# Performance work log

Measured on AMD Instinct MI355X. Metric: run time of the kernel, lower is better.

The kernel has to match this reference:

```python
import jax, jax.numpy as jnp
import numpy as np

B, R, NM, H, P1, G1, RC1, LAT = 16384, 360, 200, 256, 512, 256, 256, 128


def _linear_params(k, out_f, in_f):
    s = 1.0 / np.sqrt(in_f)
    kw, kb = jax.random.split(k)
    W = jax.random.uniform(kw, (out_f, in_f), minval=-s, maxval=s, dtype=jnp.float32)
    b = jax.random.uniform(kb, (out_f,), minval=-s, maxval=s, dtype=jnp.float32)
    return W, b


def setup_inputs() -> dict:
    key = jax.random.key(0)
    ks = jax.random.split(key, 14)
    x_window = jax.random.normal(ks[0], (B, 3, R), dtype=jnp.float32)
    modes = jax.random.normal(ks[1], (R, NM), dtype=jnp.float32)
    mode_coeff = jax.random.normal(ks[2], (B, NM), dtype=jnp.float32)
    W1, b1 = _linear_params(ks[3], H, 3 * R)      # surrogate layer 1
    W2, b2 = _linear_params(ks[4], H, H)          # surrogate layer 2
    W3, b3 = _linear_params(ks[5], R, H)          # surrogate layer 3
    Wp1, bp1 = _linear_params(ks[6], P1, R * R)   # npi_proj
    Wp2, bp2 = _linear_params(ks[7], LAT, P1)
    Wg1, bg1 = _linear_params(ks[8], G1, NM)      # geo_proj
    Wg2, bg2 = _linear_params(ks[9], LAT, G1)
    Wr1, br1 = _linear_params(ks[10], RC1, LAT)   # recon
    Wr2, br2 = _linear_params(ks[11], R, RC1)
    return dict(x_window=x_window, modes=modes, mode_coeff=mode_coeff,
                W1=W1, b1=b1, W2=W2, b2=b2, W3=W3, b3=b3,
                Wp1=Wp1, bp1=bp1, Wp2=Wp2, bp2=bp2,
                Wg1=Wg1, bg1=bg1, Wg2=Wg2, bg2=bg2,
                Wr1=Wr1, br1=br1, Wr2=Wr2, br2=br2)


def reference(x_window, modes, mode_coeff,
              W1, b1, W2, b2, W3, b3,
              Wp1, bp1, Wp2, bp2,
              Wg1, bg1, Wg2, bg2,
              Wr1, br1, Wr2, br2):
    Bs = x_window.shape[0]
    Rr = W3.shape[0]
    # ---- NPI surrogate forward (needed for ReLU masks) ----
    z = x_window.reshape(Bs, 3 * Rr)                       # (B, 3R)
    h1 = z @ W1.T + b1                                     # (B, H)
    m1 = (h1 > 0).astype(z.dtype)
    h2 = (h1 * m1) @ W2.T + b2                             # (B, H)
    m2 = (h2 > 0).astype(z.dtype)
    # ---- EC: exact batch-mean Jacobian of the ReLU MLP w.r.t last timestep ----
    # mean_b [ W3 diag(m2_b) W2 diag(m1_b) W1_last ] = W3 @ (W2 * (m2^T m1 / B)) @ W1[:, -R:]
    G = (m2.T @ m1) / Bs                                   # (H, H)
    ec = W3 @ ((W2 * G) @ W1[:, -Rr:])                     # (R, R); row j = dy_j/dx
    ec = jax.lax.stop_gradient(ec)                         # create_graph=False in original
    # ---- projections ----
    ec_flat = ec.reshape(1, Rr * Rr)
    z_npi1 = jax.nn.relu(ec_flat @ Wp1.T + bp1) @ Wp2.T + bp2   # (1, LAT)
    z_npi = jnp.tile(z_npi1, (Bs, 1))                           # (B, LAT)
    z_geo = jax.nn.relu(mode_coeff @ Wg1.T + bg1) @ Wg2.T + bg2  # (B, LAT)
    zsum = z_npi + z_geo
    zn = zsum / jnp.maximum(jnp.linalg.norm(zsum, axis=-1, keepdims=True), 1e-12)
    recon = jax.nn.relu(zn @ Wr1.T + br1) @ Wr2.T + br2          # (B, R)
    return (z_npi, z_geo, zn, ec, recon)
```

## Files before the change

### kernel.cpp

```cpp
#include <hip/hip_runtime.h>

typedef __bf16 bf16x8 __attribute__((ext_vector_type(8)));
typedef __bf16 bf16x4 __attribute__((ext_vector_type(4)));
typedef float  f32x4  __attribute__((ext_vector_type(4)));

__device__ __forceinline__ f32x4 mfma_bf16(bf16x8 a, bf16x8 b, f32x4 c) {
  return __builtin_amdgcn_mfma_f32_16x16x32_bf16(a, b, c, 0, 0, 0);
}
__device__ __forceinline__ bf16x8 ldB(const __bf16* Bp, int kt, int NT, int nt,
                                      int lane) {
  return *reinterpret_cast<const bf16x8*>(Bp + (((size_t)kt * NT + nt) * 64 + lane) * 8);
}

__device__ __forceinline__ void gridbar(int* cnt, int target) {
  __syncthreads();
  if (threadIdx.x == 0) {
    __threadfence();
    __hip_atomic_fetch_add(cnt, 1, __ATOMIC_RELEASE, __HIP_MEMORY_SCOPE_AGENT);
    while (__hip_atomic_load(cnt, __ATOMIC_RELAXED, __HIP_MEMORY_SCOPE_AGENT) < target)
      __builtin_amdgcn_s_sleep(4);
    __threadfence();
  }
  __syncthreads();
}

__global__ void pack_all(const float* __restrict__ W1, const float* __restrict__ W2,
                         const float* __restrict__ Wg1, const float* __restrict__ Wg2,
                         const float* __restrict__ Wr1, const float* __restrict__ Wr2,
                         __bf16* __restrict__ W1p, __bf16* __restrict__ W2p,
                         __bf16* __restrict__ Wg1p, __bf16* __restrict__ Wg2p,
                         __bf16* __restrict__ Wr1p, __bf16* __restrict__ Wr2p,
                         float* __restrict__ G, int* __restrict__ cnt) {
  int bx = blockIdx.x;
  int lane = threadIdx.x;
  if (bx >= 1104) {
    if (bx == 1104 && lane == 0) cnt[0] = 0;
    float4* g = (float4*)G;
    int base = (bx - 1104) * 512 + lane;
#pragma unroll
    for (int i = 0; i < 8; ++i) g[base + i * 64] = make_float4(0.f, 0.f, 0.f, 0.f);
    return;
  }
  const float* W; __bf16* out; int N, K, NT, local;
  if (bx < 544)      { W = W1;  out = W1p;  N = 256; K = 1080; NT = 16; local = bx; }
  else if (bx < 672) { W = W2;  out = W2p;  N = 256; K = 256;  NT = 16; local = bx - 544; }
  else if (bx < 784) { W = Wg1; out = Wg1p; N = 256; K = 200;  NT = 16; local = bx - 672; }
  else if (bx < 848) { W = Wg2; out = Wg2p; N = 128; K = 256;  NT = 8;  local = bx - 784; }
  else if (bx < 912) { W = Wr1; out = Wr1p; N = 256; K = 128;  NT = 16; local = bx - 848; }
  else               { W = Wr2; out = Wr2p; N = 360; K = 256;  NT = 24; local = bx - 912; }
  int nt = local % NT, kt = local / NT;
  int n = nt * 16 + (lane & 15);
  int k0 = kt * 32 + (lane >> 4) * 8;
  bf16x8 v;
#pragma unroll
  for (int e = 0; e < 8; ++e) {
    int k = k0 + e;
    float xv = (n < N && k < K) ? W[(size_t)n * K + k] : 0.f;
    v[e] = (__bf16)xv;
  }
  *reinterpret_cast<bf16x8*>(out + ((size_t)local * 64 + lane) * 8) = v;
}

__global__ __launch_bounds__(512) void h1h2_fused(
    const float* __restrict__ x, const __bf16* __restrict__ W1p,
    const float* __restrict__ b1, const __bf16* __restrict__ W2p,
    const float* __restrict__ b2, __bf16* __restrict__ m1T,
    __bf16* __restrict__ m2T) {
  __shared__ __bf16 Alds[32][68];
  __shared__ __bf16 h1s[32][264];
  int tid = threadIdx.x;
  int lane = tid & 63, wid = tid >> 6;
  int wr = wid >> 2, wc = wid & 3;
  int rowBase = blockIdx.x * 32;
  int sr = tid >> 4, sc = (tid & 15) * 4;
  const float* aSrc = x + (size_t)(rowBase + sr) * 1080;
  f32x4 acc[4] = {};
  float4 c0, c1;
  auto LD = [&](int s, float4& d) {
    int gk = s * 64 + sc;
    d = (gk < 1080) ? *(const float4*)(aSrc + gk) : make_float4(0.f, 0.f, 0.f, 0.f);
  };
  LD(0, c0);
  LD(1, c1);
  for (int s = 0; s < 17; ++s) {
    bf16x4 w4;
    w4[0] = (__bf16)c0.x; w4[1] = (__bf16)c0.y;
    w4[2] = (__bf16)c0.z; w4[3] = (__bf16)c0.w;
    *reinterpret_cast<bf16x4*>(&Alds[sr][sc]) = w4;
    __syncthreads();
    c0 = c1;
    if (s + 2 < 17) LD(s + 2, c1);
    int arow = wr * 16 + (lane & 15);
#pragma unroll
    for (int ks = 0; ks < 2; ++ks) {
      int ak = ks * 32 + (lane >> 4) * 8;
      bf16x8 a0 = *reinterpret_cast<const bf16x8*>(&Alds[arow][ak]);
      int kt = s * 2 + ks;
#pragma unroll
      for (int n = 0; n < 4; ++n) {
        bf16x8 bv = ldB(W1p, kt, 16, wc * 4 + n, lane);
        acc[n] = mfma_bf16(a0, bv, acc[n]);
      }
    }
    __syncthreads();
  }
  int q4 = (lane >> 4) * 4;
#pragma unroll
  for (int n = 0; n < 4; ++n) {
    int col = wc * 64 + n * 16 + (lane & 15);
    float bb = b1[col];
#pragma unroll
    for (int j = 0; j < 4; ++j) {
      int rl = wr * 16 + q4 + j;
      float h = acc[n][j] + bb;
      m1T[(size_t)col * 16384 + rowBase + rl] = (__bf16)(h > 0.f ? 1.f : 0.f);
      h1s[rl][col] = (__bf16)fmaxf(h, 0.f);
    }
  }
  __syncthreads();
  f32x4 acc2[4] = {};
#pragma unroll
  for (int ks = 0; ks < 8; ++ks) {
    int arow = wr * 16 + (lane & 15), ak = ks * 32 + (lane >> 4) * 8;
    bf16x8 a0 = *reinterpret_cast<const bf16x8*>(&h1s[arow][ak]);
#pragma unroll
    for (int n = 0; n < 4; ++n) {
      bf16x8 bv = ldB(W2p, ks, 16, wc * 4 + n, lane);
      acc2[n] = mfma_bf16(a0, bv, acc2[n]);
    }
  }
#pragma unroll
  for (int n = 0; n < 4; ++n) {
    int col = wc * 64 + n * 16 + (lane & 15);
    float bb = b2[col];
#pragma unroll
    for (int j = 0; j < 4; ++j) {
      int rl = wr * 16 + q4 + j;
      float h = acc2[n][j] + bb;
      m2T[(size_t)col * 16384 + rowBase + rl] = (__bf16)(h > 0.f ? 1.f : 0.f);
    }
  }
}

__global__ __launch_bounds__(256) void gemm_masks(
    const __bf16* __restrict__ m2T, const __bf16* __restrict__ m1T,
    float* __restrict__ G) {
  int tid = threadIdx.x;
  int lane = tid & 63, wid = tid >> 6;
  int wr = wid >> 1, wc = wid & 1;
  int ibase = blockIdx.x * 64, jbase = blockIdx.y * 64;
  size_t b0 = (size_t)blockIdx.z * 1024 + (lane >> 4) * 8;
  const __bf16* pa0 = m2T + (size_t)(ibase + wr * 32 + (lane & 15)) * 16384 + b0;
  const __bf16* pa1 = pa0 + (size_t)16 * 16384;
  const __bf16* pb0 = m1T + (size_t)(jbase + wc * 32 + (lane & 15)) * 16384 + b0;
  const __bf16* pb1 = pb0 + (size_t)16 * 16384;
  f32x4 acc[2][2] = {};
#pragma unroll 4
  for (int c = 0; c < 32; ++c) {
    bf16x8 a0 = *reinterpret_cast<const bf16x8*>(pa0 + c * 32);
    bf16x8 a1 = *reinterpret_cast<const bf16x8*>(pa1 + c * 32);
    bf16x8 bv0 = *reinterpret_cast<const bf16x8*>(pb0 + c * 32);
    bf16x8 bv1 = *reinterpret_cast<const bf16x8*>(pb1 + c * 32);
    acc[0][0] = mfma_bf16(a0, bv0, acc[0][0]);
    acc[0][1] = mfma_bf16(a0, bv1, acc[0][1]);
    acc[1][0] = mfma_bf16(a1, bv0, acc[1][0]);
    acc[1][1] = mfma_bf16(a1, bv1, acc[1][1]);
  }
  int q4 = (lane >> 4) * 4;
#pragma unroll
  for (int m = 0; m < 2; ++m)
#pragma unroll
    for (int n = 0; n < 2; ++n)
#pragma unroll
      for (int j = 0; j < 4; ++j) {
        int gi = ibase + wr * 32 + m * 16 + q4 + j;
        int gj = jbase + wc * 32 + n * 16 + (lane & 15);
        atomicAdd(&G[(size_t)gi * 256 + gj], acc[m][n][j] * (1.f / 16384.f));
      }
}

__device__ void small_body2(float (*As)[17], float (*Bs)[65], int t,
                            const float* __restrict__ A, const float* __restrict__ A2,
                            int lda, const float* __restrict__ Bm, int ldb,
                            bool sum4, size_t bStride, float* __restrict__ C,
                            int ldc, int M, int N, int kBeg, int kEnd,
                            int m0, int n0) {
  int tx = t & 15, ty = t >> 4;
  float acc[4][4] = {};
  for (int k0 = kBeg; k0 < kEnd; k0 += 16) {
#pragma unroll
    for (int i = 0; i < 4; ++i) {
      int idx = t * 4 + i;
      int r = idx >> 4, kk = idx & 15;
      int gm = m0 + r, gk = k0 + kk;
      float v = (gm < M) ? A[(size_t)gm * lda + gk] : 0.f;
      if (A2 && gm < M) v *= A2[(size_t)gm * lda + gk];
      As[r][kk] = v;
      int kk2 = idx >> 6, cc = idx & 63;
      int gk2 = k0 + kk2, gn = n0 + cc;
      float bv = 0.f;
      if (gn < N) {
        const float* bp = Bm + (size_t)gk2 * ldb + gn;
        bv = bp[0];
        if (sum4) bv = bv + bp[bStride] + bp[2 * bStride] + bp[3 * bStride];
      }
      Bs[kk2][cc] = bv;
    }
    __syncthreads();
#pragma unroll
    for (int kk = 0; kk < 16; ++kk)
#pragma unroll
      for (int i = 0; i < 4; ++i)
#pragma unroll
        for (int j = 0; j < 4; ++j)
          acc[i][j] += As[ty * 4 + i][kk] * Bs[kk][tx * 4 + j];
    __syncthreads();
  }
#pragma unroll
  for (int i = 0; i < 4; ++i)
#pragma unroll
    for (int j = 0; j < 4; ++j) {
      int gm = m0 + ty * 4 + i, gn = n0 + tx * 4 + j;
      if (gm < M && gn < N) C[(size_t)gm * ldc + gn] = acc[i][j];
    }
}

__global__ __launch_bounds__(256) void small_split(
    const float* __restrict__ W2, const float* __restrict__ G,
    const float* __restrict__ W1, const float* __restrict__ W3,
    float* __restrict__ Tpart, float* __restrict__ ecpart,
    float* __restrict__ o_ec, int* __restrict__ cnt) {
  __shared__ float As[64][17];
  __shared__ float Bs[16][65];
  int t = threadIdx.x, bid = blockIdx.x;
  if (bid < 96) {
    int tile = bid >> 2, kc = bid & 3;
    small_body2(As, Bs, t, W2, G, 256, W1 + 720, 1080, false, 0,
                Tpart + (size_t)kc * 98304, 384, 256, 360,
                kc * 64, kc * 64 + 64, (tile / 6) * 64, (tile % 6) * 64);
  }
  gridbar(cnt, 144);
  {
    int tile = bid >> 2, kc = bid & 3;
    small_body2(As, Bs, t, W3, nullptr, 256, Tpart, 384, true, 98304,
                ecpart + (size_t)kc * 129600, 360, 360, 360,
                kc * 64, kc * 64 + 64, (tile / 6) * 64, (tile % 6) * 64);
  }
  gridbar(cnt, 288);
  {
    int base = bid * 900;
    for (int i = t; i < 900; i += 256) {
      int idx = base + i;
      o_ec[idx] = ecpart[idx] + ecpart[129600 + idx] + ecpart[259200 + idx] +
                  ecpart[388800 + idx];
    }
  }
}

__global__ __launch_bounds__(512) void p_and_g1(
    const float* __restrict__ Wp1, const float* __restrict__ ec,
    const float* __restrict__ bp1, float* __restrict__ p,
    const float* __restrict__ mc, const __bf16* __restrict__ Wg1p,
    const float* __restrict__ bg1, const __bf16* __restrict__ Wg2p,
    const float* __restrict__ bg2, float* __restrict__ o_zgeo) {
  __shared__ __bf16 Alds[64][40];
  __shared__ __bf16 g1S[64][264];
  __shared__ float redw[8];
  int t = threadIdx.x;
  if (blockIdx.x < 512) {
    int row = blockIdx.x;
    const float4* w = (const float4*)(Wp1 + (size_t)row * 129600);
    const float4* e = (const float4*)ec;
    float s = 0.f;
    for (int i = t; i < 32400; i += 512) {
      float4 a = w[i], b = e[i];
      s += a.x * b.x + a.y * b.y + a.z * b.z + a.w * b.w;
    }
    for (int o = 32; o; o >>= 1) s += __shfl_down(s, o);
    if ((t & 63) == 0) redw[t >> 6] = s;
    __syncthreads();
    if (t == 0) {
      float tot = 0.f;
#pragma unroll
      for (int i = 0; i < 8; ++i) tot += redw[i];
      p[row] = fmaxf(tot + bp1[row], 0.f);
    }
  } else {
    int lane = t & 63, wid = t >> 6;
    int wr = wid >> 2, wc = wid & 3;
    int rowBase = (blockIdx.x - 512) * 64;
    int sr = t >> 3, sc = (t & 7) * 4;
    const float* aSrc = mc + (size_t)(rowBase + sr) * 200;
    int q4 = (lane >> 4) * 4;
    f32x4 acc[2][4] = {};
    for (int kt = 0; kt < 7; ++kt) {
      int gk = kt * 32 + sc;
      bf16x4 w4;
      if (gk < 200) {
        float4 v = *(const float4*)(aSrc + gk);
        w4[0] = (__bf16)v.x; w4[1] = (__bf16)v.y;
        w4[2] = (__bf16)v.z; w4[3] = (__bf16)v.w;
      } else {
        w4[0] = w4[1] = w4[2] = w4[3] = (__bf16)0.f;
      }
      *reinterpret_cast<bf16x4*>(&Alds[sr][sc]) = w4;
      __syncthreads();
      int arow = wr * 32 + (lane & 15), ak = (lane >> 4) * 8;
      bf16x8 a0 = *reinterpret_cast<const bf16x8*>(&Alds[arow][ak]);
      bf16x8 a1 = *reinterpret_cast<const bf16x8*>(&Alds[arow + 16][ak]);
#pragma unroll
      for (int n = 0; n < 4; ++n) {
        bf16x8 bv = ldB(Wg1p, kt, 16, wc * 4 + n, lane);
        acc[0][n] = mfma_bf16(a0, bv, acc[0][n]);
        acc[1][n] = mfma_bf16(a1, bv, acc[1][n]);
      }
      __syncthreads();
    }
#pragma unroll
    for (int m = 0; m < 2; ++m)
#pragma unroll
      for (int n = 0; n < 4; ++n) {
        int col = wc * 64 + n * 16 + (lane & 15);
        float bb = bg1[col];
#pragma unroll
        for (int j = 0; j < 4; ++j) {
          int rl = wr * 32 + m * 16 + q4 + j;
          g1S[rl][col] = (__bf16)fmaxf(acc[m][n][j] + bb, 0.f);
        }
      }
    __syncthreads();
    f32x4 acc2[2][2] = {};
#pragma unroll
    for (int ks = 0; ks < 8; ++ks) {
      int arow = wr * 32 + (lane & 15), ak = ks * 32 + (lane >> 4) * 8;
      bf16x8 a0 = *reinterpret_cast<const bf16x8*>(&g1S[arow][ak]);
      bf16x8 a1 = *reinterpret_cast<const bf16x8*>(&g1S[arow + 16][ak]);
#pragma unroll
      for (int n = 0; n < 2; ++n) {
        bf16x8 bv = ldB(Wg2p, ks, 8, wc * 2 + n, lane);
        acc2[0][n] = mfma_bf16(a0, bv, acc2[0][n]);
        acc2[1][n] = mfma_bf16(a1, bv, acc2[1][n]);
      }
    }
#pragma unroll
    for (int m = 0; m < 2; ++m)
#pragma unroll
      for (int n = 0; n < 2; ++n) {
        int col = wc * 32 + n * 16 + (lane & 15);
        float bb = bg2[col];
#pragma unroll
        for (int j = 0; j < 4; ++j) {
          int row = rowBase + wr * 32 + m * 16 + q4 + j;
          o_zgeo[(size_t)row * 128 + col] = acc2[m][n][j] + bb;
        }
      }
  }
}

__global__ void gemv_z(const float* __restrict__ p, const float* __restrict__ Wp2,
                       const float* __restrict__ bp2, float* __restrict__ znpi1) {
  int j = blockIdx.x;
  int t = threadIdx.x;
  const float4* w = (const float4*)(Wp2 + (size_t)j * 512);
  const float4* pp = (const float4*)p;
  float4 a0 = w[t], b0 = pp[t];
  float4 a1 = w[t + 64], b1 = pp[t + 64];
  float s = a0.x * b0.x + a0.y * b0.y + a0.z * b0.z + a0.w * b0.w +
            a1.x * b1.x + a1.y * b1.y + a1.z * b1.z + a1.w * b1.w;
  for (int o = 32; o; o >>= 1) s += __shfl_down(s, o);
  if (t == 0) znpi1[j] = s + bp2[j];
}

__global__ __launch_bounds__(512) void mega_tail(
    const float* __restrict__ zgeo, const float* __restrict__ znpi1,
    const __bf16* __restrict__ Wr1p, const float* __restrict__ br1,
    const __bf16* __restrict__ Wr2p, const float* __restrict__ br2,
    float* __restrict__ o_znpi, float* __restrict__ o_zn,
    float* __restrict__ o_rec) {
  __shared__ __bf16 r1S[64][264];
  __shared__ __bf16 znS[64][136];
  __shared__ float znpiS[128];
  int tid = threadIdx.x;
  int lane = tid & 63, wid = tid >> 6;
  int wr = wid >> 2, wc = wid & 3;
  int rowBase = blockIdx.x * 64;
  int q4 = (lane >> 4) * 4;
  if (tid < 128) znpiS[tid] = znpi1[tid];
  __syncthreads();
  {
    int rg = tid >> 5;
    int c4 = (tid & 31) * 4;
    float4 zp = make_float4(znpiS[c4], znpiS[c4 + 1], znpiS[c4 + 2], znpiS[c4 + 3]);
#pragma unroll
    for (int ri = 0; ri < 4; ++ri) {
      int rl = rg + ri * 16;
      int row = rowBase + rl;
      float4 zg = *(const float4*)(zgeo + (size_t)row * 128 + c4);
      float4 zs = make_float4(zg.x + zp.x, zg.y + zp.y, zg.z + zp.z, zg.w + zp.w);
      *(float4*)(o_znpi + (size_t)row * 128 + c4) = zp;
      float ss = zs.x * zs.x + zs.y * zs.y + zs.z * zs.z + zs.w * zs.w;
      ss += __shfl_xor(ss, 1);
      ss += __shfl_xor(ss, 2);
      ss += __shfl_xor(ss, 4);
      ss += __shfl_xor(ss, 8);
      ss += __shfl_xor(ss, 16);
      float rn = 1.f / fmaxf(sqrtf(ss), 1e-12f);
      float4 zn = make_float4(zs.x * rn, zs.y * rn, zs.z * rn, zs.w * rn);
      *(float4*)(o_zn + (size_t)row * 128 + c4) = zn;
      bf16x4 znb;
      znb[0] = (__bf16)zn.x; znb[1] = (__bf16)zn.y;
      znb[2] = (__bf16)zn.z; znb[3] = (__bf16)zn.w;
      *reinterpret_cast<bf16x4*>(&znS[rl][c4]) = znb;
    }
  }
  __syncthreads();
  {
    f32x4 acc[2][4] = {};
#pragma unroll
    for (int ks = 0; ks < 4; ++ks) {
      int arow = wr * 32 + (lane & 15), ak = ks * 32 + (lane >> 4) * 8;
      bf16x8 a0 = *reinterpret_cast<const bf16x8*>(&znS[arow][ak]);
      bf16x8 a1 = *reinterpret_cast<const bf16x8*>(&znS[arow + 16][ak]);
#pragma unroll
      for (int n = 0; n < 4; ++n) {
        bf16x8 bv = ldB(Wr1p, ks, 16, wc * 4 + n, lane);
        acc[0][n] = mfma_bf16(a0, bv, acc[0][n]);
        acc[1][n] = mfma_bf16(a1, bv, acc[1][n]);
      }
    }
#pragma unroll
    for (int m = 0; m < 2; ++m)
#pragma unroll
      for (int n = 0; n < 4; ++n) {
        int col = wc * 64 + n * 16 + (lane & 15);
        float bb = br1[col];
#pragma unroll
        for (int j = 0; j < 4; ++j) {
          int rl = wr * 32 + m * 16 + q4 + j;
          r1S[rl][col] = (__bf16)fmaxf(acc[m][n][j] + bb, 0.f);
        }
      }
  }
  __syncthreads();
  {
    f32x4 acc[2][6] = {};
#pragma unroll
    for (int ks = 0; ks < 8; ++ks) {
      int arow = wr * 32 + (lane & 15), ak = ks * 32 + (lane >> 4) * 8;
      bf16x8 a0 = *reinterpret_cast<const bf16x8*>(&r1S[arow][ak]);
      bf16x8 a1 = *reinterpret_cast<const bf16x8*>(&r1S[arow + 16][ak]);
#pragma unroll
      for (int n = 0; n < 6; ++n) {
        bf16x8 bv = ldB(Wr2p, ks, 24, wc * 6 + n, lane);
        acc[0][n] = mfma_bf16(a0, bv, acc[0][n]);
        acc[1][n] = mfma_bf16(a1, bv, acc[1][n]);
      }
    }
#pragma unroll
    for (int m = 0; m < 2; ++m)
#pragma unroll
      for (int n = 0; n < 6; ++n) {
        int col = wc * 96 + n * 16 + (lane & 15);
        if (col < 360) {
          float bb = br2[col];
#pragma unroll
          for (int j = 0; j < 4; ++j) {
            int rl = wr * 32 + m * 16 + q4 + j;
            o_rec[(size_t)(rowBase + rl) * 360 + col] = acc[m][n][j] + bb;
          }
        }
      }
  }
}

extern "C" void kernel_launch(void* const* d_in, const int* in_sizes, int n_in,
                              void* d_out, int out_size, void* d_ws,
                              size_t ws_size, hipStream_t stream) {
  (void)in_sizes; (void)n_in; (void)out_size; (void)ws_size;
  const float* x   = (const float*)d_in[0];
  const float* mc  = (const float*)d_in[2];
  const float* W1  = (const float*)d_in[3];  const float* b1  = (const float*)d_in[4];
  const float* W2  = (const float*)d_in[5];  const float* b2  = (const float*)d_in[6];
  const float* W3  = (const float*)d_in[7];
  const float* Wp1 = (const float*)d_in[9];  const float* bp1 = (const float*)d_in[10];
  const float* Wp2 = (const float*)d_in[11]; const float* bp2 = (const float*)d_in[12];
  const float* Wg1 = (const float*)d_in[13]; const float* bg1 = (const float*)d_in[14];
  const float* Wg2 = (const float*)d_in[15]; const float* bg2 = (const float*)d_in[16];
  const float* Wr1 = (const float*)d_in[17]; const float* br1 = (const float*)d_in[18];
  const float* Wr2 = (const float*)d_in[19]; const float* br2 = (const float*)d_in[20];

  float* out = (float*)d_out;
  float* o_znpi = out;
  float* o_zgeo = out + 2097152;
  float* o_zn   = out + 4194304;
  float* o_ec   = out + 6291456;
  float* o_rec  = out + 6421056;

  char* ws = (char*)d_ws;
  __bf16* m1T    = (__bf16*)(ws + 0);
  __bf16* m2T    = (__bf16*)(ws + 8388608);
  float*  G      = (float*)(ws + 16777216);
  float*  Tpart  = (float*)(ws + 17039360);
  float*  ecpart = (float*)(ws + 18612224);
  float*  p512   = (float*)(ws + 20686848);
  float*  znpi1  = (float*)(ws + 20688896);
  __bf16* W1p    = (__bf16*)(ws + 20689920);
  __bf16* W2p    = W1p  + (size_t)544 * 512;
  __bf16* Wg1p   = W2p  + (size_t)128 * 512;
  __bf16* Wg2p   = Wg1p + (size_t)112 * 512;
  __bf16* Wr1p   = Wg2p + (size_t)64 * 512;
  __bf16* Wr2p   = Wr1p + (size_t)64 * 512;
  int*    cnt    = (int*)(ws + 22020096);

  pack_all<<<1136, 64, 0, stream>>>(W1, W2, Wg1, Wg2, Wr1, Wr2,
                                    W1p, W2p, Wg1p, Wg2p, Wr1p, Wr2p, G, cnt);
  h1h2_fused<<<512, 512, 0, stream>>>(x, W1p, b1, W2p, b2, m1T, m2T);
  gemm_masks<<<dim3(4, 4, 16), 256, 0, stream>>>(m2T, m1T, G);
  small_split<<<144, 256, 0, stream>>>(W2, G, W1, W3, Tpart, ecpart, o_ec, cnt);
  p_and_g1<<<768, 512, 0, stream>>>(Wp1, o_ec, bp1, p512, mc, Wg1p, bg1,
                                    Wg2p, bg2, o_zgeo);
  gemv_z<<<128, 64, 0, stream>>>(p512, Wp2, bp2, znpi1);
  mega_tail<<<256, 512, 0, stream>>>(o_zgeo, znpi1, Wr1p, br1, Wr2p, br2,
                                     o_znpi, o_zn, o_rec);
}
```

Baseline: 221.6 us.

## Fuse mask GEMM into EC kernel and fold Wp2 GEMV into last p block

The separate gemm_masks launch is merged into the EC kernel as a first phase, with an extra grid barrier before the small GEMM phases; the grid grows to 256 blocks. The gemv_z kernel is removed, and the last-finishing block of the Wp1 projection, found through an atomic counter, computes the 128-output GEMV. This removes two kernel launches and their gaps. The cost is an extra grid-wide barrier, and the design relies on all 256 blocks being co-resident and on a second counter reset in pack_all.

```diff
diff --git a/kernel.cpp b/kernel.cpp
--- a/kernel.cpp
+++ b/kernel.cpp
@@ -34,7 +34,7 @@
   int bx = blockIdx.x;
   int lane = threadIdx.x;
   if (bx >= 1104) {
-    if (bx == 1104 && lane == 0) cnt[0] = 0;
+    if (bx == 1104 && lane < 2) cnt[lane] = 0;
     float4* g = (float4*)G;
     int base = (bx - 1104) * 512 + lane;
 #pragma unroll
@@ -142,43 +142,6 @@
   }
 }
 
-__global__ __launch_bounds__(256) void gemm_masks(
-    const __bf16* __restrict__ m2T, const __bf16* __restrict__ m1T,
-    float* __restrict__ G) {
-  int tid = threadIdx.x;
-  int lane = tid & 63, wid = tid >> 6;
-  int wr = wid >> 1, wc = wid & 1;
-  int ibase = blockIdx.x * 64, jbase = blockIdx.y * 64;
-  size_t b0 = (size_t)blockIdx.z * 1024 + (lane >> 4) * 8;
-  const __bf16* pa0 = m2T + (size_t)(ibase + wr * 32 + (lane & 15)) * 16384 + b0;
-  const __bf16* pa1 = pa0 + (size_t)16 * 16384;
-  const __bf16* pb0 = m1T + (size_t)(jbase + wc * 32 + (lane & 15)) * 16384 + b0;
-  const __bf16* pb1 = pb0 + (size_t)16 * 16384;
-  f32x4 acc[2][2] = {};
-#pragma unroll 4
-  for (int c = 0; c < 32; ++c) {
-    bf16x8 a0 = *reinterpret_cast<const bf16x8*>(pa0 + c * 32);
-    bf16x8 a1 = *reinterpret_cast<const bf16x8*>(pa1 + c * 32);
-    bf16x8 bv0 = *reinterpret_cast<const bf16x8*>(pb0 + c * 32);
-    bf16x8 bv1 = *reinterpret_cast<const bf16x8*>(pb1 + c * 32);
-    acc[0][0] = mfma_bf16(a0, bv0, acc[0][0]);
-    acc[0][1] = mfma_bf16(a0, bv1, acc[0][1]);
-    acc[1][0] = mfma_bf16(a1, bv0, acc[1][0]);
-    acc[1][1] = mfma_bf16(a1, bv1, acc[1][1]);
-  }
-  int q4 = (lane >> 4) * 4;
-#pragma unroll
-  for (int m = 0; m < 2; ++m)
-#pragma unroll
-    for (int n = 0; n < 2; ++n)
-#pragma unroll
-      for (int j = 0; j < 4; ++j) {
-        int gi = ibase + wr * 32 + m * 16 + q4 + j;
-        int gj = jbase + wc * 32 + n * 16 + (lane & 15);
-        atomicAdd(&G[(size_t)gi * 256 + gj], acc[m][n][j] * (1.f / 16384.f));
-      }
-}
-
 __device__ void small_body2(float (*As)[17], float (*Bs)[65], int t,
                             const float* __restrict__ A, const float* __restrict__ A2,
                             int lda, const float* __restrict__ Bm, int ldb,
@@ -225,31 +188,68 @@
     }
 }
 
-__global__ __launch_bounds__(256) void small_split(
-    const float* __restrict__ W2, const float* __restrict__ G,
-    const float* __restrict__ W1, const float* __restrict__ W3,
+__global__ __launch_bounds__(256) void masks_ec(
+    const __bf16* __restrict__ m2T, const __bf16* __restrict__ m1T,
+    float* __restrict__ G,
+    const float* __restrict__ W2, const float* __restrict__ W1,
+    const float* __restrict__ W3,
     float* __restrict__ Tpart, float* __restrict__ ecpart,
     float* __restrict__ o_ec, int* __restrict__ cnt) {
   __shared__ float As[64][17];
   __shared__ float Bs[16][65];
-  int t = threadIdx.x, bid = blockIdx.x;
+  int tid = threadIdx.x, bid = blockIdx.x;
+  {
+    int lane = tid & 63, wid = tid >> 6;
+    int wr = wid >> 1, wc = wid & 1;
+    int ij = bid & 15;
+    int ibase = (ij >> 2) * 64, jbase = (ij & 3) * 64;
+    size_t b0 = (size_t)(bid >> 4) * 1024 + (lane >> 4) * 8;
+    const __bf16* pa0 = m2T + (size_t)(ibase + wr * 32 + (lane & 15)) * 16384 + b0;
+    const __bf16* pa1 = pa0 + (size_t)16 * 16384;
+    const __bf16* pb0 = m1T + (size_t)(jbase + wc * 32 + (lane & 15)) * 16384 + b0;
+    const __bf16* pb1 = pb0 + (size_t)16 * 16384;
+    f32x4 acc[2][2] = {};
+#pragma unroll 4
+    for (int c = 0; c < 32; ++c) {
+      bf16x8 a0 = *reinterpret_cast<const bf16x8*>(pa0 + c * 32);
+      bf16x8 a1 = *reinterpret_cast<const bf16x8*>(pa1 + c * 32);
+      bf16x8 bv0 = *reinterpret_cast<const bf16x8*>(pb0 + c * 32);
+      bf16x8 bv1 = *reinterpret_cast<const bf16x8*>(pb1 + c * 32);
+      acc[0][0] = mfma_bf16(a0, bv0, acc[0][0]);
+      acc[0][1] = mfma_bf16(a0, bv1, acc[0][1]);
+      acc[1][0] = mfma_bf16(a1, bv0, acc[1][0]);
+      acc[1][1] = mfma_bf16(a1, bv1, acc[1][1]);
+    }
+    int q4 = (lane >> 4) * 4;
+#pragma unroll
+    for (int m = 0; m < 2; ++m)
+#pragma unroll
+      for (int n = 0; n < 2; ++n)
+#pragma unroll
+        for (int j = 0; j < 4; ++j) {
+          int gi = ibase + wr * 32 + m * 16 + q4 + j;
+          int gj = jbase + wc * 32 + n * 16 + (lane & 15);
+          atomicAdd(&G[(size_t)gi * 256 + gj], acc[m][n][j] * (1.f / 16384.f));
+        }
+  }
+  gridbar(cnt, 256);
   if (bid < 96) {
     int tile = bid >> 2, kc = bid & 3;
-    small_body2(As, Bs, t, W2, G, 256, W1 + 720, 1080, false, 0,
+    small_body2(As, Bs, tid, W2, G, 256, W1 + 720, 1080, false, 0,
                 Tpart + (size_t)kc * 98304, 384, 256, 360,
                 kc * 64, kc * 64 + 64, (tile / 6) * 64, (tile % 6) * 64);
   }
-  gridbar(cnt, 144);
-  {
+  gridbar(cnt, 512);
+  if (bid < 144) {
     int tile = bid >> 2, kc = bid & 3;
-    small_body2(As, Bs, t, W3, nullptr, 256, Tpart, 384, true, 98304,
+    small_body2(As, Bs, tid, W3, nullptr, 256, Tpart, 384, true, 98304,
                 ecpart + (size_t)kc * 129600, 360, 360, 360,
                 kc * 64, kc * 64 + 64, (tile / 6) * 64, (tile % 6) * 64);
   }
-  gridbar(cnt, 288);
-  {
+  gridbar(cnt, 768);
+  if (bid < 144) {
     int base = bid * 900;
-    for (int i = t; i < 900; i += 256) {
+    for (int i = tid; i < 900; i += 256) {
       int idx = base + i;
       o_ec[idx] = ecpart[idx] + ecpart[129600 + idx] + ecpart[259200 + idx] +
                   ecpart[388800 + idx];
@@ -260,12 +260,15 @@
 __global__ __launch_bounds__(512) void p_and_g1(
     const float* __restrict__ Wp1, const float* __restrict__ ec,
     const float* __restrict__ bp1, float* __restrict__ p,
+    const float* __restrict__ Wp2, const float* __restrict__ bp2,
+    float* __restrict__ znpi1, int* __restrict__ pdone,
     const float* __restrict__ mc, const __bf16* __restrict__ Wg1p,
     const float* __restrict__ bg1, const __bf16* __restrict__ Wg2p,
     const float* __restrict__ bg2, float* __restrict__ o_zgeo) {
   __shared__ __bf16 Alds[64][40];
   __shared__ __bf16 g1S[64][264];
   __shared__ float redw[8];
+  __shared__ int lastFlag;
   int t = threadIdx.x;
   if (blockIdx.x < 512) {
     int row = blockIdx.x;
@@ -284,6 +287,27 @@
 #pragma unroll
       for (int i = 0; i < 8; ++i) tot += redw[i];
       p[row] = fmaxf(tot + bp1[row], 0.f);
+      __threadfence();
+      int old = __hip_atomic_fetch_add(pdone, 1, __ATOMIC_ACQ_REL,
+                                       __HIP_MEMORY_SCOPE_AGENT);
+      lastFlag = (old == 511);
+    }
+    __syncthreads();
+    if (lastFlag) {
+      __threadfence();
+      int lane = t & 63, wv = t >> 6;
+      const float4* pp = (const float4*)p;
+      float4 b0 = pp[lane], b1 = pp[lane + 64];
+#pragma unroll
+      for (int jj = 0; jj < 16; ++jj) {
+        int j = wv * 16 + jj;
+        const float4* wq = (const float4*)(Wp2 + (size_t)j * 512);
+        float4 a0 = wq[lane], a1 = wq[lane + 64];
+        float s = a0.x * b0.x + a0.y * b0.y + a0.z * b0.z + a0.w * b0.w +
+                  a1.x * b1.x + a1.y * b1.y + a1.z * b1.z + a1.w * b1.w;
+        for (int o = 32; o; o >>= 1) s += __shfl_down(s, o);
+        if (lane == 0) znpi1[j] = s + bp2[j];
+      }
     }
   } else {
     int lane = t & 63, wid = t >> 6;
@@ -355,20 +379,6 @@
         }
       }
   }
-}
-
-__global__ void gemv_z(const float* __restrict__ p, const float* __restrict__ Wp2,
-                       const float* __restrict__ bp2, float* __restrict__ znpi1) {
-  int j = blockIdx.x;
-  int t = threadIdx.x;
-  const float4* w = (const float4*)(Wp2 + (size_t)j * 512);
-  const float4* pp = (const float4*)p;
-  float4 a0 = w[t], b0 = pp[t];
-  float4 a1 = w[t + 64], b1 = pp[t + 64];
-  float s = a0.x * b0.x + a0.y * b0.y + a0.z * b0.z + a0.w * b0.w +
-            a1.x * b1.x + a1.y * b1.y + a1.z * b1.z + a1.w * b1.w;
-  for (int o = 32; o; o >>= 1) s += __shfl_down(s, o);
-  if (t == 0) znpi1[j] = s + bp2[j];
 }
 
 __global__ __launch_bounds__(512) void mega_tail(
@@ -515,11 +525,10 @@
   pack_all<<<1136, 64, 0, stream>>>(W1, W2, Wg1, Wg2, Wr1, Wr2,
                                     W1p, W2p, Wg1p, Wg2p, Wr1p, Wr2p, G, cnt);
   h1h2_fused<<<512, 512, 0, stream>>>(x, W1p, b1, W2p, b2, m1T, m2T);
-  gemm_masks<<<dim3(4, 4, 16), 256, 0, stream>>>(m2T, m1T, G);
-  small_split<<<144, 256, 0, stream>>>(W2, G, W1, W3, Tpart, ecpart, o_ec, cnt);
-  p_and_g1<<<768, 512, 0, stream>>>(Wp1, o_ec, bp1, p512, mc, Wg1p, bg1,
-                                    Wg2p, bg2, o_zgeo);
-  gemv_z<<<128, 64, 0, stream>>>(p512, Wp2, bp2, znpi1);
+  masks_ec<<<256, 256, 0, stream>>>(m2T, m1T, G, W2, W1, W3, Tpart, ecpart,
+                                    o_ec, cnt);
+  p_and_g1<<<768, 512, 0, stream>>>(Wp1, o_ec, bp1, p512, Wp2, bp2, znpi1,
+                                    cnt + 1, mc, Wg1p, bg1, Wg2p, bg2, o_zgeo);
   mega_tail<<<256, 512, 0, stream>>>(o_zgeo, znpi1, Wr1p, br1, Wr2p, br2,
                                      o_znpi, o_zn, o_rec);
 }
```

Result: slower. 311.6 us (+40.6%).

## Stage ec vector in LDS and process four Wp1 rows per block

Applied to the files above, without the earlier changes.

The Wp1 GEMV now has each block handle four output rows, with two waves per row. The ec vector is staged once per chunk into shared memory and reused by all four rows instead of being re-read from global memory for every row. This cuts the p-part grid from 512 blocks to 128, so the launch drops from 768 to 384 blocks. Global ec traffic falls, but each chunk adds two barriers and fewer blocks stream the 265MB Wp1 matrix, which may lower the achieved memory bandwidth.

```diff
diff --git a/kernel.cpp b/kernel.cpp
--- a/kernel.cpp
+++ b/kernel.cpp
@@ -34,7 +34,7 @@
   int bx = blockIdx.x;
   int lane = threadIdx.x;
   if (bx >= 1104) {
-    if (bx == 1104 && lane == 0) cnt[0] = 0;
+    if (bx == 1104 && lane < 2) cnt[lane] = 0;
     float4* g = (float4*)G;
     int base = (bx - 1104) * 512 + lane;
 #pragma unroll
@@ -263,32 +263,60 @@
     const float* __restrict__ mc, const __bf16* __restrict__ Wg1p,
     const float* __restrict__ bg1, const __bf16* __restrict__ Wg2p,
     const float* __restrict__ bg2, float* __restrict__ o_zgeo) {
-  __shared__ __bf16 Alds[64][40];
-  __shared__ __bf16 g1S[64][264];
-  __shared__ float redw[8];
+  __shared__ __align__(16) char SM[39424];
   int t = threadIdx.x;
-  if (blockIdx.x < 512) {
-    int row = blockIdx.x;
-    const float4* w = (const float4*)(Wp1 + (size_t)row * 129600);
-    const float4* e = (const float4*)ec;
+  if (blockIdx.x < 128) {
+    float4* eS = (float4*)SM;
+    float* sred = (float*)(SM + 32768);
+    int lane = t & 63, w = t >> 6;
+    int row = blockIdx.x * 4 + (w & 3);
+    int half = w >> 2;
+    const float4* wrow = (const float4*)(Wp1 + (size_t)row * 129600);
+    const float4* e4 = (const float4*)ec;
     float s = 0.f;
-    for (int i = t; i < 32400; i += 512) {
-      float4 a = w[i], b = e[i];
-      s += a.x * b.x + a.y * b.y + a.z * b.z + a.w * b.w;
+    for (int c = 0; c < 15; ++c) {
+      int base = c * 2048;
+      __syncthreads();
+#pragma unroll
+      for (int k = 0; k < 4; ++k) eS[t + 512 * k] = e4[base + t + 512 * k];
+      __syncthreads();
+#pragma unroll
+      for (int j = 0; j < 16; ++j) {
+        int li = lane + 64 * (half * 16 + j);
+        float4 a = wrow[base + li], b = eS[li];
+        s += a.x * b.x + a.y * b.y + a.z * b.z + a.w * b.w;
+      }
+    }
+    {
+      int base = 30720;
+      __syncthreads();
+#pragma unroll
+      for (int k = 0; k < 4; ++k) {
+        int idx = base + t + 512 * k;
+        if (idx < 32400) eS[t + 512 * k] = e4[idx];
+      }
+      __syncthreads();
+#pragma unroll
+      for (int j = 0; j < 16; ++j) {
+        int li = lane + 64 * (half * 16 + j);
+        int idx = base + li;
+        if (idx < 32400) {
+          float4 a = wrow[idx], b = eS[li];
+          s += a.x * b.x + a.y * b.y + a.z * b.z + a.w * b.w;
+        }
+      }
     }
     for (int o = 32; o; o >>= 1) s += __shfl_down(s, o);
-    if ((t & 63) == 0) redw[t >> 6] = s;
+    if (lane == 0) sred[w] = s;
     __syncthreads();
-    if (t == 0) {
-      float tot = 0.f;
-#pragma unroll
-      for (int i = 0; i < 8; ++i) tot += redw[i];
-      p[row] = fmaxf(tot + bp1[row], 0.f);
-    }
+    if (t < 4)
+      p[blockIdx.x * 4 + t] = fmaxf(sred[t] + sred[t + 4] + bp1[blockIdx.x * 4 + t], 0.f);
   } else {
+    __bf16 (*Alds)[40] = (__bf16(*)[40])SM;
+    __bf16 (*g1S)[264] = (__bf16(*)[264])(SM + 5120);
     int lane = t & 63, wid = t >> 6;
     int wr = wid >> 2, wc = wid & 3;
-    int rowBase = (blockIdx.x - 512) * 64;
+    int rowBase = (blockIdx.x - 128) * 64;
     int sr = t >> 3, sc = (t & 7) * 4;
     const float* aSrc = mc + (size_t)(rowBase + sr) * 200;
     int q4 = (lane >> 4) * 4;
@@ -516,8 +544,9 @@
                                     W1p, W2p, Wg1p, Wg2p, Wr1p, Wr2p, G, cnt);
   h1h2_fused<<<512, 512, 0, stream>>>(x, W1p, b1, W2p, b2, m1T, m2T);
   gemm_masks<<<dim3(4, 4, 16), 256, 0, stream>>>(m2T, m1T, G);
-  small_split<<<144, 256, 0, stream>>>(W2, G, W1, W3, Tpart, ecpart, o_ec, cnt);
-  p_and_g1<<<768, 512, 0, stream>>>(Wp1, o_ec, bp1, p512, mc, Wg1p, bg1,
+  small_split<<<144, 256, 0, stream>>>(W2, G, W1, W3, Tpart, ecpart, o_ec,
+                                       cnt);
+  p_and_g1<<<384, 512, 0, stream>>>(Wp1, o_ec, bp1, p512, mc, Wg1p, bg1,
                                     Wg2p, bg2, o_zgeo);
   gemv_z<<<128, 64, 0, stream>>>(p512, Wp2, bp2, znpi1);
   mega_tail<<<256, 512, 0, stream>>>(o_zgeo, znpi1, Wr1p, br1, Wr2p, br2,
```

After: 244.6 us. +10.4%, slower.

## Split Wp1 GEMV into per-wave segments with partial sums reduced in gemv_z

Applied to the files above, without the earlier changes.

The Wp1·ec GEMV now gives each wavefront a quarter-row segment, so 256 blocks replace 512 and there is no block-level LDS reduction or __syncthreads. Four partial sums per row are written to workspace. gemv_z reduces them, adds the bias and applies ReLU into shared memory before its dot product. The g1 branch shares one LDS buffer, and a second counter slot is zeroed. The aim is better load balance and fewer blocks on the bandwidth-bound Wp1 read, at the cost of redundant partial-sum reduction in each gemv_z block.

```diff
diff --git a/kernel.cpp b/kernel.cpp
--- a/kernel.cpp
+++ b/kernel.cpp
@@ -34,7 +34,7 @@
   int bx = blockIdx.x;
   int lane = threadIdx.x;
   if (bx >= 1104) {
-    if (bx == 1104 && lane == 0) cnt[0] = 0;
+    if (bx == 1104 && lane < 2) cnt[lane] = 0;
     float4* g = (float4*)G;
     int base = (bx - 1104) * 512 + lane;
 #pragma unroll
@@ -259,36 +259,33 @@
 
 __global__ __launch_bounds__(512) void p_and_g1(
     const float* __restrict__ Wp1, const float* __restrict__ ec,
-    const float* __restrict__ bp1, float* __restrict__ p,
+    float* __restrict__ pPart,
     const float* __restrict__ mc, const __bf16* __restrict__ Wg1p,
     const float* __restrict__ bg1, const __bf16* __restrict__ Wg2p,
     const float* __restrict__ bg2, float* __restrict__ o_zgeo) {
-  __shared__ __bf16 Alds[64][40];
-  __shared__ __bf16 g1S[64][264];
-  __shared__ float redw[8];
+  __shared__ __align__(16) char SM[39424];
   int t = threadIdx.x;
-  if (blockIdx.x < 512) {
-    int row = blockIdx.x;
-    const float4* w = (const float4*)(Wp1 + (size_t)row * 129600);
-    const float4* e = (const float4*)ec;
+  if (blockIdx.x < 256) {
+    int lane = t & 63, w = t >> 6;
+    int task = blockIdx.x * 8 + w;
+    int row = task >> 2;
+    int seg = task & 3;
+    const float4* wseg = (const float4*)(Wp1 + (size_t)row * 129600) + seg * 8100;
+    const float4* eseg = (const float4*)ec + seg * 8100;
     float s = 0.f;
-    for (int i = t; i < 32400; i += 512) {
-      float4 a = w[i], b = e[i];
+#pragma unroll 4
+    for (int i = lane; i < 8100; i += 64) {
+      float4 a = wseg[i], b = eseg[i];
       s += a.x * b.x + a.y * b.y + a.z * b.z + a.w * b.w;
     }
     for (int o = 32; o; o >>= 1) s += __shfl_down(s, o);
-    if ((t & 63) == 0) redw[t >> 6] = s;
-    __syncthreads();
-    if (t == 0) {
-      float tot = 0.f;
-#pragma unroll
-      for (int i = 0; i < 8; ++i) tot += redw[i];
-      p[row] = fmaxf(tot + bp1[row], 0.f);
-    }
+    if (lane == 0) pPart[seg * 512 + row] = s;
   } else {
+    __bf16 (*Alds)[40] = (__bf16(*)[40])SM;
+    __bf16 (*g1S)[264] = (__bf16(*)[264])(SM + 5120);
     int lane = t & 63, wid = t >> 6;
     int wr = wid >> 2, wc = wid & 3;
-    int rowBase = (blockIdx.x - 512) * 64;
+    int rowBase = (blockIdx.x - 256) * 64;
     int sr = t >> 3, sc = (t & 7) * 4;
     const float* aSrc = mc + (size_t)(rowBase + sr) * 200;
     int q4 = (lane >> 4) * 4;
@@ -357,12 +354,23 @@
   }
 }
 
-__global__ void gemv_z(const float* __restrict__ p, const float* __restrict__ Wp2,
-                       const float* __restrict__ bp2, float* __restrict__ znpi1) {
+__global__ void gemv_z(const float* __restrict__ pPart,
+                       const float* __restrict__ bp1,
+                       const float* __restrict__ Wp2,
+                       const float* __restrict__ bp2,
+                       float* __restrict__ znpi1) {
+  __shared__ __align__(16) float pS[512];
   int j = blockIdx.x;
   int t = threadIdx.x;
+#pragma unroll
+  for (int r0 = 0; r0 < 512; r0 += 64) {
+    int r = r0 + t;
+    float v = pPart[r] + pPart[512 + r] + pPart[1024 + r] + pPart[1536 + r];
+    pS[r] = fmaxf(v + bp1[r], 0.f);
+  }
+  __syncthreads();
   const float4* w = (const float4*)(Wp2 + (size_t)j * 512);
-  const float4* pp = (const float4*)p;
+  const float4* pp = (const float4*)pS;
   float4 a0 = w[t], b0 = pp[t];
   float4 a1 = w[t + 64], b1 = pp[t + 64];
   float s = a0.x * b0.x + a0.y * b0.y + a0.z * b0.z + a0.w * b0.w +
@@ -502,9 +510,9 @@
   float*  G      = (float*)(ws + 16777216);
   float*  Tpart  = (float*)(ws + 17039360);
   float*  ecpart = (float*)(ws + 18612224);
-  float*  p512   = (float*)(ws + 20686848);
-  float*  znpi1  = (float*)(ws + 20688896);
-  __bf16* W1p    = (__bf16*)(ws + 20689920);
+  float*  pPart  = (float*)(ws + 20686848);
+  float*  znpi1  = (float*)(ws + 20695040);
+  __bf16* W1p    = (__bf16*)(ws + 20695552);
   __bf16* W2p    = W1p  + (size_t)544 * 512;
   __bf16* Wg1p   = W2p  + (size_t)128 * 512;
   __bf16* Wg2p   = Wg1p + (size_t)112 * 512;
@@ -516,10 +524,11 @@
                                     W1p, W2p, Wg1p, Wg2p, Wr1p, Wr2p, G, cnt);
   h1h2_fused<<<512, 512, 0, stream>>>(x, W1p, b1, W2p, b2, m1T, m2T);
   gemm_masks<<<dim3(4, 4, 16), 256, 0, stream>>>(m2T, m1T, G);
-  small_split<<<144, 256, 0, stream>>>(W2, G, W1, W3, Tpart, ecpart, o_ec, cnt);
-  p_and_g1<<<768, 512, 0, stream>>>(Wp1, o_ec, bp1, p512, mc, Wg1p, bg1,
+  small_split<<<144, 256, 0, stream>>>(W2, G, W1, W3, Tpart, ecpart, o_ec,
+                                       cnt);
+  p_and_g1<<<512, 512, 0, stream>>>(Wp1, o_ec, pPart, mc, Wg1p, bg1,
                                     Wg2p, bg2, o_zgeo);
-  gemv_z<<<128, 64, 0, stream>>>(p512, Wp2, bp2, znpi1);
+  gemv_z<<<128, 64, 0, stream>>>(pPart, bp1, Wp2, bp2, znpi1);
   mega_tail<<<256, 512, 0, stream>>>(o_zgeo, znpi1, Wr1p, br1, Wr2p, br2,
                                      o_znpi, o_zn, o_rec);
 }
```

Result: no change. 225.1 us (+1.6%).
